# Performance work log

Measured on AMD Instinct MI355X. Metric: run time of the kernel, lower is better.

## Reference

```python
import jax, jax.numpy as jnp
import numpy as np

B, N = 256, 65536          # batch, num_tokens (world.num_tokens == N)
VOCAB = 50257
ALPHA = 0.5                # dirichlet concentration
EPS = 1e-7                 # gumbel eps


def setup_inputs() -> dict:
    key = jax.random.key(0)
    kb, kt, ku, kd = jax.random.split(key, 4)
    batch = jax.random.randint(kb, (B, N), 0, VOCAB, dtype=jnp.int32)
    t = jax.random.uniform(kt, (B,), dtype=jnp.float32)
    U = jax.random.uniform(ku, (B, N), dtype=jnp.float32)
    # dirichlet(alpha=0.5) sample over the token axis, one simplex per row
    D = jax.random.dirichlet(kd, ALPHA * jnp.ones((N,), jnp.float32), shape=(B,)).astype(jnp.float32)
    return {"batch": batch, "t": t, "U": U, "D": D}


def cosine_schedule(t):
    return 1.0 - jnp.cos(jnp.pi * t / 2)


def cosine_weight(t, eps=1e-3):
    t_adj = t * (1 - 2 * eps) + eps
    return 0.5 * jnp.pi * jnp.sin(jnp.pi * t_adj / 2)


def binary_topk(weights, ks):
    # weights: [B, N] float; ks: [B, 1] int -> bool mask marking the top-k per row
    Bn, Nn = weights.shape
    idx = jnp.argsort(-weights, axis=-1)                     # descending order indices
    rank = jnp.broadcast_to(jnp.arange(Nn), (Bn, Nn))        # rank of each sorted slot
    mask = jnp.zeros((Bn, Nn), dtype=bool)
    mask = mask.at[jnp.arange(Bn)[:, None], idx].set(ks > rank)
    return mask


def reference(batch, t, U, D):
    r = cosine_schedule(t)                                   # mask rate per sample [B]
    w = cosine_weight(t)                                     # loss weight per sample [B]
    G = -jnp.log(-jnp.log(U + EPS) + EPS)                    # gumbel noise [B, N]
    weights = G + jnp.log(D)                                 # gumbel + log-dirichlet
    ks = (N * r).astype(jnp.int32)[:, None]                  # [B, 1] tokens to mask
    mask = binary_topk(weights, ks)                          # [B, N] bool
    return mask, w
```

## Files before the change

kernel.cpp:

```cpp
#include <hip/hip_runtime.h>
#include <math.h>

#define BB 256
#define NN 65536
#define NT 1024
#define CAP 6144
#define MARGIN 2e-3f

typedef float f32x4 __attribute__((ext_vector_type(4)));

__device__ __forceinline__ unsigned int f2sort(float f) {
    unsigned int b = __float_as_uint(f);
    return (b & 0x80000000u) ? ~b : (b | 0x80000000u);
}
__device__ __forceinline__ float sort2f(unsigned int u) {
    unsigned int b = (u & 0x80000000u) ? (u & 0x7fffffffu) : ~u;
    return __uint_as_float(b);
}

__device__ __forceinline__ unsigned int wexact(float u, float d) {
    float t1 = u + 1e-7f;
    float t2 = (float)log((double)t1);
    float t3 = (-t2) + 1e-7f;
    float G  = -(float)log((double)t3);
    float lgD = (float)log((double)d);
    return f2sort(G + lgD);
}

__device__ __forceinline__ unsigned int wfast(float u, float d) {
    float t1 = u + 1e-7f;
    float t3 = -__logf(t1) + 1e-7f;
    float G  = -__logf(t3);
    return f2sort(G + __logf(d));
}

__device__ __forceinline__ bool finite_f(float f) {
    return (__float_as_uint(f) & 0x7f800000u) != 0x7f800000u;
}

#define CHUNKS(OP) OP(0) OP(1) OP(2) OP(3) OP(4) OP(5) OP(6) OP(7) \
                   OP(8) OP(9) OP(10) OP(11) OP(12) OP(13) OP(14) OP(15)

#define PASS1SEL(KKV) \
    { const int b0 = tid * 8; unsigned int cs = 0; \
      _Pragma("unroll") for (int i = 0; i < 8; i++) cs += hist[b0 + i]; \
      chunkSum[tid] = cs; } \
    __syncthreads(); \
    if (tid < 64) { \
        const int c0i = lane * 16; unsigned int s = 0; \
        _Pragma("unroll") for (int i = 0; i < 16; i++) s += chunkSum[c0i + i]; \
        unsigned int suf = s; \
        _Pragma("unroll") for (int off = 1; off < 64; off <<= 1) { \
            unsigned int tv = __shfl_down(suf, off); if (lane + off < 64) suf += tv; } \
        unsigned int above = suf - s; \
        if (suf >= (KKV) && above < (KKV)) { \
            unsigned int cum = above; \
            for (int ci = c0i + 15; ci >= c0i; ci--) { \
                unsigned int cch = chunkSum[ci]; \
                if (cum + cch >= (KKV)) { \
                    for (int b = ci * 8 + 7; ; b--) { \
                        unsigned int c2 = hist[b]; \
                        if (cum + c2 >= (KKV)) { s_sel = (unsigned int)b; s_kneed = (KKV) - cum; s_eq = c2; break; } \
                        cum += c2; } \
                    break; } \
                cum += cch; } } } \
    __syncthreads();

#define PASS2SEL(P, KN) \
    if (tid < 64) { \
        const int c0i = lane * 16; unsigned int s = 0; \
        _Pragma("unroll") for (int i = 0; i < 16; i++) s += hist[c0i + i]; \
        unsigned int suf = s; \
        _Pragma("unroll") for (int off = 1; off < 64; off <<= 1) { \
            unsigned int tv = __shfl_down(suf, off); if (lane + off < 64) suf += tv; } \
        unsigned int above = suf - s; \
        if (suf >= (KN) && above < (KN)) { \
            unsigned int cum = above; \
            for (int b = c0i + 15; ; b--) { \
                unsigned int c2 = hist[b]; \
                if (cum + c2 >= (KN)) { s_sel = ((P) << 10) | (unsigned int)b; s_kneed = (KN) - cum; s_eq = c2; break; } \
                cum += c2; } } } \
    __syncthreads();

#define PASS3SEL(P, KN) \
    if (tid < 64) { \
        const int c0i = lane * 8; unsigned int s = 0; \
        _Pragma("unroll") for (int i = 0; i < 8; i++) s += hist[c0i + i]; \
        unsigned int suf = s; \
        _Pragma("unroll") for (int off = 1; off < 64; off <<= 1) { \
            unsigned int tv = __shfl_down(suf, off); if (lane + off < 64) suf += tv; } \
        unsigned int above = suf - s; \
        if (suf >= (KN) && above < (KN)) { \
            unsigned int cum = above; \
            for (int b = c0i + 7; ; b--) { \
                unsigned int c2 = hist[b]; \
                if (cum + c2 >= (KN)) { s_sel = ((P) << 9) | (unsigned int)b; s_kneed = (KN) - cum; s_eq = c2; break; } \
                cum += c2; } } } \
    __syncthreads();

__global__ __launch_bounds__(NT, 4)
void md_fused_kernel(const float* __restrict__ Tt,
                     const float* __restrict__ U,
                     const float* __restrict__ D,
                     float* __restrict__ out,
                     float* __restrict__ wout) {
    const int row = blockIdx.x;
    const int tid = threadIdx.x;
    const int lane = tid & 63;

    const float* Ur = U + (size_t)row * NN;
    const float* Dr = D + (size_t)row * NN;
    float* Or = out + (size_t)row * NN;

    __shared__ unsigned int hist[8192];
    __shared__ unsigned int chunkSum[NT];
    __shared__ unsigned int bandU[CAP];
    __shared__ int bandIdx[CAP];
    __shared__ int s_tielist[1024];
    __shared__ unsigned int s_sel, s_kneed, s_eq;
    __shared__ int s_A, s_bandCnt, s_tiecnt, s_tieidx;

    const float t = Tt[row];
    const float pf = (float)M_PI;
    float aa = pf * t;
    float bbv = aa * 0.5f;
    float c0 = (float)cos((double)bbv);
    float r  = 1.0f - c0;
    const int k = (int)(65536.0f * r);
    if (tid == 0) {
        float tadj = t * 0.998f + 0.001f;
        float arg  = (pf * tadj) * 0.5f;
        wout[row] = (float)(0.5 * M_PI) * (float)sin((double)arg);
    }

    if (k <= 0 || k >= NN) {
        const float fill = (k >= NN) ? 1.0f : 0.0f;
        f32x4 f4 = {fill, fill, fill, fill};
        for (int j = 0; j < 16; j++)
            __builtin_nontemporal_store(f4, (f32x4*)(Or + j * 4096 + tid * 4));
        return;
    }
    const unsigned int kk = (unsigned int)k;

    uint4 v0, v1, v2, v3, v4, v5, v6, v7, v8, v9, v10, v11, v12, v13, v14, v15;

    for (int i = tid; i < 8192; i += NT) hist[i] = 0;
    if (tid == 0) { s_A = 0; s_bandCnt = 0; }
    __syncthreads();

#define COMPF(J) { \
        int e = (J) * 4096 + tid * 4; \
        float4 u4 = *(const float4*)(Ur + e); \
        float4 d4 = *(const float4*)(Dr + e); \
        v##J.x = wfast(u4.x, d4.x); \
        v##J.y = wfast(u4.y, d4.y); \
        v##J.z = wfast(u4.z, d4.z); \
        v##J.w = wfast(u4.w, d4.w); \
        atomicAdd(&hist[v##J.x >> 19], 1u); \
        atomicAdd(&hist[v##J.y >> 19], 1u); \
        atomicAdd(&hist[v##J.z >> 19], 1u); \
        atomicAdd(&hist[v##J.w >> 19], 1u); }
    CHUNKS(COMPF)
#undef COMPF
    __syncthreads();

    PASS1SEL(kk)
    const unsigned int p13 = s_sel;
    const unsigned int kn1 = s_kneed;
    hist[tid] = 0;
    __syncthreads();
#define P2F(J) { \
        if ((v##J.x >> 19) == p13) atomicAdd(&hist[(v##J.x >> 9) & 1023u], 1u); \
        if ((v##J.y >> 19) == p13) atomicAdd(&hist[(v##J.y >> 9) & 1023u], 1u); \
        if ((v##J.z >> 19) == p13) atomicAdd(&hist[(v##J.z >> 9) & 1023u], 1u); \
        if ((v##J.w >> 19) == p13) atomicAdd(&hist[(v##J.w >> 9) & 1023u], 1u); }
    CHUNKS(P2F)
#undef P2F
    __syncthreads();
    PASS2SEL(p13, kn1)

    const unsigned int p23 = s_sel;
    const float loF = sort2f(p23 << 9) - MARGIN;
    const float hiF = sort2f((p23 << 9) | 511u) + MARGIN;
    const bool badBand = !(finite_f(loF) && finite_f(hiF));
    const unsigned int lo_u = f2sort(loF);
    const unsigned int hi_u = f2sort(hiF);

    {
        int cnt = 0;
#define MRG1(J, C, CI, MF) { const unsigned int uu = v##J.C; \
        const bool din = uu > hi_u; cnt += (int)din; MF = din ? 1.0f : 0.0f; \
        if (!din && uu >= lo_u) { \
            int slot = atomicAdd(&s_bandCnt, 1); \
            if (slot < CAP) bandIdx[slot] = (J) * 4096 + tid * 4 + (CI); } }
#define MRG(J) { const int e = (J) * 4096 + tid * 4; f32x4 m; \
        MRG1(J, x, 0, m.x) MRG1(J, y, 1, m.y) MRG1(J, z, 2, m.z) MRG1(J, w, 3, m.w) \
        __builtin_nontemporal_store(m, (f32x4*)(Or + e)); }
        CHUNKS(MRG)
#undef MRG
#undef MRG1
#pragma unroll
        for (int off = 32; off >= 1; off >>= 1) cnt += __shfl_down(cnt, off);
        if (lane == 0) atomicAdd(&s_A, cnt);
    }
    __syncthreads();

    const int bandCnt = s_bandCnt;
    const int kb = k - s_A;
    const bool fallback = badBand || (bandCnt > CAP) || (kb < 0) || (kb > bandCnt);

    if (!fallback) {
        for (int j = tid; j < bandCnt; j += NT) {
            int idx = bandIdx[j];
            bandU[j] = wexact(Ur[idx], Dr[idx]);
        }
        __syncthreads();
        for (int j = tid; j < bandCnt; j += NT) {
            unsigned int me = bandU[j];
            int mi = bandIdx[j];
            int rk = 0;
            for (int i = 0; i < bandCnt; i++) {
                unsigned int o = bandU[i];
                rk += (int)((o > me) || (o == me && bandIdx[i] < mi));
            }
            if (rk < kb) Or[mi] = 1.0f;
        }
        return;
    }

    __syncthreads();
    for (int i = tid; i < 8192; i += NT) hist[i] = 0;
    __syncthreads();
#define COMPE(J) { \
        int e = (J) * 4096 + tid * 4; \
        float4 u4 = *(const float4*)(Ur + e); \
        float4 d4 = *(const float4*)(Dr + e); \
        v##J.x = wexact(u4.x, d4.x); \
        v##J.y = wexact(u4.y, d4.y); \
        v##J.z = wexact(u4.z, d4.z); \
        v##J.w = wexact(u4.w, d4.w); \
        atomicAdd(&hist[v##J.x >> 19], 1u); \
        atomicAdd(&hist[v##J.y >> 19], 1u); \
        atomicAdd(&hist[v##J.z >> 19], 1u); \
        atomicAdd(&hist[v##J.w >> 19], 1u); }
    CHUNKS(COMPE)
#undef COMPE
    __syncthreads();

    PASS1SEL(kk)
    const unsigned int q13 = s_sel;
    const unsigned int en1 = s_kneed;
    hist[tid] = 0;
    __syncthreads();
#define P2E(J) { \
        if ((v##J.x >> 19) == q13) atomicAdd(&hist[(v##J.x >> 9) & 1023u], 1u); \
        if ((v##J.y >> 19) == q13) atomicAdd(&hist[(v##J.y >> 9) & 1023u], 1u); \
        if ((v##J.z >> 19) == q13) atomicAdd(&hist[(v##J.z >> 9) & 1023u], 1u); \
        if ((v##J.w >> 19) == q13) atomicAdd(&hist[(v##J.w >> 9) & 1023u], 1u); }
    CHUNKS(P2E)
#undef P2E
    __syncthreads();
    PASS2SEL(q13, en1)

    const unsigned int q23 = s_sel;
    const unsigned int en2 = s_kneed;
    if (tid < 512) hist[tid] = 0;
    __syncthreads();
#define P3E(J) { \
        if ((v##J.x >> 9) == q23) atomicAdd(&hist[v##J.x & 511u], 1u); \
        if ((v##J.y >> 9) == q23) atomicAdd(&hist[v##J.y & 511u], 1u); \
        if ((v##J.z >> 9) == q23) atomicAdd(&hist[v##J.z & 511u], 1u); \
        if ((v##J.w >> 9) == q23) atomicAdd(&hist[v##J.w & 511u], 1u); }
    CHUNKS(P3E)
#undef P3E
    __syncthreads();
    PASS3SEL(q23, en2)

    const unsigned int theta = s_sel;
    const unsigned int kneedF = s_kneed, eqF = s_eq;
    const bool needOrder = (kneedF < eqF);
    int istar = NN;
    if (needOrder) {
        if (tid == 0) s_tiecnt = 0;
        __syncthreads();
#define TIE1(J, C, CI) if (v##J.C == theta) { \
            int pos = atomicAdd(&s_tiecnt, 1); \
            if (pos < 1024) s_tielist[pos] = (J) * 4096 + tid * 4 + (CI); }
#define TIE(J) TIE1(J, x, 0) TIE1(J, y, 1) TIE1(J, z, 2) TIE1(J, w, 3)
        CHUNKS(TIE)
#undef TIE
#undef TIE1
        __syncthreads();
        if (tid == 0) {
            int E = s_tiecnt; if (E > 1024) E = 1024;
            for (int aI = 1; aI < E; aI++) {
                int val = s_tielist[aI]; int bI = aI - 1;
                while (bI >= 0 && s_tielist[bI] > val) { s_tielist[bI + 1] = s_tielist[bI]; bI--; }
                s_tielist[bI + 1] = val;
            }
            int kk2 = (int)kneedF; if (kk2 > E) kk2 = E; if (kk2 < 1) kk2 = 1;
            s_tieidx = s_tielist[kk2 - 1];
        }
        __syncthreads();
        istar = s_tieidx;
    }

#define MVE(u, idx) ((((u) > theta) || ((u) == theta && (!needOrder || (idx) <= istar))) ? 1.0f : 0.0f)
#define WRE(J) { \
        int e = (J) * 4096 + tid * 4; \
        f32x4 m; \
        m.x = MVE(v##J.x, e + 0); \
        m.y = MVE(v##J.y, e + 1); \
        m.z = MVE(v##J.z, e + 2); \
        m.w = MVE(v##J.w, e + 3); \
        __builtin_nontemporal_store(m, (f32x4*)(Or + e)); }
    CHUNKS(WRE)
#undef WRE
#undef MVE
}

extern "C" void kernel_launch(void* const* d_in, const int* in_sizes, int n_in,
                              void* d_out, int out_size, void* d_ws, size_t ws_size,
                              hipStream_t stream) {
    const float* T = (const float*)d_in[1];
    const float* U = (const float*)d_in[2];
    const float* D = (const float*)d_in[3];
    float* out = (float*)d_out;
    float* wout = out + (size_t)BB * NN;

    md_fused_kernel<<<BB, NT, 0, stream>>>(T, U, D, out, wout);
}
```

Before: 231.7 us.

## Spill seven key chunks to LDS to cut register pressure

Keeps 7 of the 16 per-thread uint4 key chunks in shared memory instead of registers, so fewer VGPRs are live across the selection passes. The band and tie buffers are shrunk or aliased onto that shared region to stay within the LDS budget. The goal is to lower register pressure or spilling at 1024 threads per block, at the cost of extra LDS traffic on every pass and a smaller band capacity (CAP 2016), which makes the slow exact fallback path trigger more often.

```diff
diff --git a/kernel.cpp b/kernel.cpp
--- a/kernel.cpp
+++ b/kernel.cpp
@@ -4,8 +4,9 @@
 #define BB 256
 #define NN 65536
 #define NT 1024
-#define CAP 6144
+#define CAP 2016
 #define MARGIN 2e-3f
+#define NLC 7
 
 typedef float f32x4 __attribute__((ext_vector_type(4)));
 
@@ -38,8 +39,8 @@
     return (__float_as_uint(f) & 0x7f800000u) != 0x7f800000u;
 }
 
-#define CHUNKS(OP) OP(0) OP(1) OP(2) OP(3) OP(4) OP(5) OP(6) OP(7) \
-                   OP(8) OP(9) OP(10) OP(11) OP(12) OP(13) OP(14) OP(15)
+#define LCHUNKS(OP) OP(0) OP(1) OP(2) OP(3) OP(4) OP(5) OP(6)
+#define RCHUNKS(OP) OP(7) OP(8) OP(9) OP(10) OP(11) OP(12) OP(13) OP(14) OP(15)
 
 #define PASS1SEL(KKV) \
     { const int b0 = tid * 8; unsigned int cs = 0; \
@@ -112,13 +113,15 @@
     const float* Dr = D + (size_t)row * NN;
     float* Or = out + (size_t)row * NN;
 
+    __shared__ uint4 kls[NLC * 1024];
     __shared__ unsigned int hist[8192];
     __shared__ unsigned int chunkSum[NT];
-    __shared__ unsigned int bandU[CAP];
     __shared__ int bandIdx[CAP];
-    __shared__ int s_tielist[1024];
     __shared__ unsigned int s_sel, s_kneed, s_eq;
     __shared__ int s_A, s_bandCnt, s_tiecnt, s_tieidx;
+
+    unsigned int* bandU = (unsigned int*)kls;
+    int* tielist = bandIdx;
 
     const float t = Tt[row];
     const float pf = (float)M_PI;
@@ -142,13 +145,29 @@
     }
     const unsigned int kk = (unsigned int)k;
 
-    uint4 v0, v1, v2, v3, v4, v5, v6, v7, v8, v9, v10, v11, v12, v13, v14, v15;
+    uint4 v7, v8, v9, v10, v11, v12, v13, v14, v15;
 
     for (int i = tid; i < 8192; i += NT) hist[i] = 0;
     if (tid == 0) { s_A = 0; s_bandCnt = 0; }
     __syncthreads();
 
-#define COMPF(J) { \
+#define COMPFL(J) { \
+        int e = (J) * 4096 + tid * 4; \
+        float4 u4 = *(const float4*)(Ur + e); \
+        float4 d4 = *(const float4*)(Dr + e); \
+        uint4 kv; \
+        kv.x = wfast(u4.x, d4.x); \
+        kv.y = wfast(u4.y, d4.y); \
+        kv.z = wfast(u4.z, d4.z); \
+        kv.w = wfast(u4.w, d4.w); \
+        kls[(J) * 1024 + tid] = kv; \
+        atomicAdd(&hist[kv.x >> 19], 1u); \
+        atomicAdd(&hist[kv.y >> 19], 1u); \
+        atomicAdd(&hist[kv.z >> 19], 1u); \
+        atomicAdd(&hist[kv.w >> 19], 1u); }
+    LCHUNKS(COMPFL)
+#undef COMPFL
+#define COMPFR(J) { \
         int e = (J) * 4096 + tid * 4; \
         float4 u4 = *(const float4*)(Ur + e); \
         float4 d4 = *(const float4*)(Dr + e); \
@@ -160,8 +179,8 @@
         atomicAdd(&hist[v##J.y >> 19], 1u); \
         atomicAdd(&hist[v##J.z >> 19], 1u); \
         atomicAdd(&hist[v##J.w >> 19], 1u); }
-    CHUNKS(COMPF)
-#undef COMPF
+    RCHUNKS(COMPFR)
+#undef COMPFR
     __syncthreads();
 
     PASS1SEL(kk)
@@ -169,13 +188,15 @@
     const unsigned int kn1 = s_kneed;
     hist[tid] = 0;
     __syncthreads();
-#define P2F(J) { \
-        if ((v##J.x >> 19) == p13) atomicAdd(&hist[(v##J.x >> 9) & 1023u], 1u); \
-        if ((v##J.y >> 19) == p13) atomicAdd(&hist[(v##J.y >> 9) & 1023u], 1u); \
-        if ((v##J.z >> 19) == p13) atomicAdd(&hist[(v##J.z >> 9) & 1023u], 1u); \
-        if ((v##J.w >> 19) == p13) atomicAdd(&hist[(v##J.w >> 9) & 1023u], 1u); }
-    CHUNKS(P2F)
-#undef P2F
+#define P2V(UU) if (((UU) >> 19) == p13) atomicAdd(&hist[((UU) >> 9) & 1023u], 1u);
+#define P2FL(J) { const uint4 kv = kls[(J) * 1024 + tid]; \
+        P2V(kv.x) P2V(kv.y) P2V(kv.z) P2V(kv.w) }
+#define P2FR(J) { P2V(v##J.x) P2V(v##J.y) P2V(v##J.z) P2V(v##J.w) }
+    LCHUNKS(P2FL)
+    RCHUNKS(P2FR)
+#undef P2FL
+#undef P2FR
+#undef P2V
     __syncthreads();
     PASS2SEL(p13, kn1)
 
@@ -188,17 +209,25 @@
 
     {
         int cnt = 0;
-#define MRG1(J, C, CI, MF) { const unsigned int uu = v##J.C; \
+#define MRGV(UU, EIDX, MF) { const unsigned int uu = (UU); \
         const bool din = uu > hi_u; cnt += (int)din; MF = din ? 1.0f : 0.0f; \
         if (!din && uu >= lo_u) { \
             int slot = atomicAdd(&s_bandCnt, 1); \
-            if (slot < CAP) bandIdx[slot] = (J) * 4096 + tid * 4 + (CI); } }
-#define MRG(J) { const int e = (J) * 4096 + tid * 4; f32x4 m; \
-        MRG1(J, x, 0, m.x) MRG1(J, y, 1, m.y) MRG1(J, z, 2, m.z) MRG1(J, w, 3, m.w) \
+            if (slot < CAP) bandIdx[slot] = (EIDX); } }
+#define MRGL(J) { const int e = (J) * 4096 + tid * 4; \
+        const uint4 kv = kls[(J) * 1024 + tid]; f32x4 m; \
+        MRGV(kv.x, e + 0, m.x) MRGV(kv.y, e + 1, m.y) \
+        MRGV(kv.z, e + 2, m.z) MRGV(kv.w, e + 3, m.w) \
         __builtin_nontemporal_store(m, (f32x4*)(Or + e)); }
-        CHUNKS(MRG)
-#undef MRG
-#undef MRG1
+#define MRGR(J) { const int e = (J) * 4096 + tid * 4; f32x4 m; \
+        MRGV(v##J.x, e + 0, m.x) MRGV(v##J.y, e + 1, m.y) \
+        MRGV(v##J.z, e + 2, m.z) MRGV(v##J.w, e + 3, m.w) \
+        __builtin_nontemporal_store(m, (f32x4*)(Or + e)); }
+        LCHUNKS(MRGL)
+        RCHUNKS(MRGR)
+#undef MRGL
+#undef MRGR
+#undef MRGV
 #pragma unroll
         for (int off = 32; off >= 1; off >>= 1) cnt += __shfl_down(cnt, off);
         if (lane == 0) atomicAdd(&s_A, cnt);
@@ -231,7 +260,23 @@
     __syncthreads();
     for (int i = tid; i < 8192; i += NT) hist[i] = 0;
     __syncthreads();
-#define COMPE(J) { \
+#define COMPEL(J) { \
+        int e = (J) * 4096 + tid * 4; \
+        float4 u4 = *(const float4*)(Ur + e); \
+        float4 d4 = *(const float4*)(Dr + e); \
+        uint4 kv; \
+        kv.x = wexact(u4.x, d4.x); \
+        kv.y = wexact(u4.y, d4.y); \
+        kv.z = wexact(u4.z, d4.z); \
+        kv.w = wexact(u4.w, d4.w); \
+        kls[(J) * 1024 + tid] = kv; \
+        atomicAdd(&hist[kv.x >> 19], 1u); \
+        atomicAdd(&hist[kv.y >> 19], 1u); \
+        atomicAdd(&hist[kv.z >> 19], 1u); \
+        atomicAdd(&hist[kv.w >> 19], 1u); }
+    LCHUNKS(COMPEL)
+#undef COMPEL
+#define COMPER(J) { \
         int e = (J) * 4096 + tid * 4; \
         float4 u4 = *(const float4*)(Ur + e); \
         float4 d4 = *(const float4*)(Dr + e); \
@@ -243,8 +288,8 @@
         atomicAdd(&hist[v##J.y >> 19], 1u); \
         atomicAdd(&hist[v##J.z >> 19], 1u); \
         atomicAdd(&hist[v##J.w >> 19], 1u); }
-    CHUNKS(COMPE)
-#undef COMPE
+    RCHUNKS(COMPER)
+#undef COMPER
     __syncthreads();
 
     PASS1SEL(kk)
@@ -252,13 +297,15 @@
     const unsigned int en1 = s_kneed;
     hist[tid] = 0;
     __syncthreads();
-#define P2E(J) { \
-        if ((v##J.x >> 19) == q13) atomicAdd(&hist[(v##J.x >> 9) & 1023u], 1u); \
-        if ((v##J.y >> 19) == q13) atomicAdd(&hist[(v##J.y >> 9) & 1023u], 1u); \
-        if ((v##J.z >> 19) == q13) atomicAdd(&hist[(v##J.z >> 9) & 1023u], 1u); \
-        if ((v##J.w >> 19) == q13) atomicAdd(&hist[(v##J.w >> 9) & 1023u], 1u); }
-    CHUNKS(P2E)
-#undef P2E
+#define P2V(UU) if (((UU) >> 19) == q13) atomicAdd(&hist[((UU) >> 9) & 1023u], 1u);
+#define P2EL(J) { const uint4 kv = kls[(J) * 1024 + tid]; \
+        P2V(kv.x) P2V(kv.y) P2V(kv.z) P2V(kv.w) }
+#define P2ER(J) { P2V(v##J.x) P2V(v##J.y) P2V(v##J.z) P2V(v##J.w) }
+    LCHUNKS(P2EL)
+    RCHUNKS(P2ER)
+#undef P2EL
+#undef P2ER
+#undef P2V
     __syncthreads();
     PASS2SEL(q13, en1)
 
@@ -266,13 +313,15 @@
     const unsigned int en2 = s_kneed;
     if (tid < 512) hist[tid] = 0;
     __syncthreads();
-#define P3E(J) { \
-        if ((v##J.x >> 9) == q23) atomicAdd(&hist[v##J.x & 511u], 1u); \
-        if ((v##J.y >> 9) == q23) atomicAdd(&hist[v##J.y & 511u], 1u); \
-        if ((v##J.z >> 9) == q23) atomicAdd(&hist[v##J.z & 511u], 1u); \
-        if ((v##J.w >> 9) == q23) atomicAdd(&hist[v##J.w & 511u], 1u); }
-    CHUNKS(P3E)
-#undef P3E
+#define P3V(UU) if (((UU) >> 9) == q23) atomicAdd(&hist[(UU) & 511u], 1u);
+#define P3EL(J) { const uint4 kv = kls[(J) * 1024 + tid]; \
+        P3V(kv.x) P3V(kv.y) P3V(kv.z) P3V(kv.w) }
+#define P3ER(J) { P3V(v##J.x) P3V(v##J.y) P3V(v##J.z) P3V(v##J.w) }
+    LCHUNKS(P3EL)
+    RCHUNKS(P3ER)
+#undef P3EL
+#undef P3ER
+#undef P3V
     __syncthreads();
     PASS3SEL(q23, en2)
 
@@ -283,39 +332,52 @@
     if (needOrder) {
         if (tid == 0) s_tiecnt = 0;
         __syncthreads();
-#define TIE1(J, C, CI) if (v##J.C == theta) { \
+#define TIEV(UU, EIDX) if ((UU) == theta) { \
             int pos = atomicAdd(&s_tiecnt, 1); \
-            if (pos < 1024) s_tielist[pos] = (J) * 4096 + tid * 4 + (CI); }
-#define TIE(J) TIE1(J, x, 0) TIE1(J, y, 1) TIE1(J, z, 2) TIE1(J, w, 3)
-        CHUNKS(TIE)
-#undef TIE
-#undef TIE1
+            if (pos < 1024) tielist[pos] = (EIDX); }
+#define TIEL(J) { const int e = (J) * 4096 + tid * 4; \
+        const uint4 kv = kls[(J) * 1024 + tid]; \
+        TIEV(kv.x, e + 0) TIEV(kv.y, e + 1) TIEV(kv.z, e + 2) TIEV(kv.w, e + 3) }
+#define TIER(J) { const int e = (J) * 4096 + tid * 4; \
+        TIEV(v##J.x, e + 0) TIEV(v##J.y, e + 1) TIEV(v##J.z, e + 2) TIEV(v##J.w, e + 3) }
+        LCHUNKS(TIEL)
+        RCHUNKS(TIER)
+#undef TIEL
+#undef TIER
+#undef TIEV
         __syncthreads();
         if (tid == 0) {
             int E = s_tiecnt; if (E > 1024) E = 1024;
             for (int aI = 1; aI < E; aI++) {
-                int val = s_tielist[aI]; int bI = aI - 1;
-                while (bI >= 0 && s_tielist[bI] > val) { s_tielist[bI + 1] = s_tielist[bI]; bI--; }
-                s_tielist[bI + 1] = val;
+                int val = tielist[aI]; int bI = aI - 1;
+                while (bI >= 0 && tielist[bI] > val) { tielist[bI + 1] = tielist[bI]; bI--; }
+                tielist[bI + 1] = val;
             }
             int kk2 = (int)kneedF; if (kk2 > E) kk2 = E; if (kk2 < 1) kk2 = 1;
-            s_tieidx = s_tielist[kk2 - 1];
+            s_tieidx = tielist[kk2 - 1];
         }
         __syncthreads();
         istar = s_tieidx;
     }
 
 #define MVE(u, idx) ((((u) > theta) || ((u) == theta && (!needOrder || (idx) <= istar))) ? 1.0f : 0.0f)
-#define WRE(J) { \
-        int e = (J) * 4096 + tid * 4; \
-        f32x4 m; \
+#define WREL(J) { const int e = (J) * 4096 + tid * 4; \
+        const uint4 kv = kls[(J) * 1024 + tid]; f32x4 m; \
+        m.x = MVE(kv.x, e + 0); \
+        m.y = MVE(kv.y, e + 1); \
+        m.z = MVE(kv.z, e + 2); \
+        m.w = MVE(kv.w, e + 3); \
+        __builtin_nontemporal_store(m, (f32x4*)(Or + e)); }
+#define WRER(J) { const int e = (J) * 4096 + tid * 4; f32x4 m; \
         m.x = MVE(v##J.x, e + 0); \
         m.y = MVE(v##J.y, e + 1); \
         m.z = MVE(v##J.z, e + 2); \
         m.w = MVE(v##J.w, e + 3); \
         __builtin_nontemporal_store(m, (f32x4*)(Or + e)); }
-    CHUNKS(WRE)
-#undef WRE
+    LCHUNKS(WREL)
+    RCHUNKS(WRER)
+#undef WREL
+#undef WRER
 #undef MVE
 }
 
```

After: 223.4 us. 3.6% less time.

## Keep 7 of 16 key chunks in LDS and recompute the rest

Applied to the files above, without the earlier changes.

Sort keys were previously held in 64 registers per thread. Now the first 7 chunks are cached in shared memory and the other 9 are recomputed from U and D in each later pass. The band capacity shrinks and the tie list reuses the band index buffer, so the total fits in LDS. This lowers register pressure so more waves can be resident, at the cost of re-reading global memory and recomputing logs in every pass. Occupancy stays capped by the large LDS footprint, and overflowing the smaller band capacity sends more rows to the slow exact fallback.

```diff
diff --git a/kernel.cpp b/kernel.cpp
--- a/kernel.cpp
+++ b/kernel.cpp
@@ -4,8 +4,9 @@
 #define BB 256
 #define NN 65536
 #define NT 1024
-#define CAP 6144
+#define CAP 2016
 #define MARGIN 2e-3f
+#define NLC 7
 
 typedef float f32x4 __attribute__((ext_vector_type(4)));
 
@@ -37,9 +38,6 @@
 __device__ __forceinline__ bool finite_f(float f) {
     return (__float_as_uint(f) & 0x7f800000u) != 0x7f800000u;
 }
-
-#define CHUNKS(OP) OP(0) OP(1) OP(2) OP(3) OP(4) OP(5) OP(6) OP(7) \
-                   OP(8) OP(9) OP(10) OP(11) OP(12) OP(13) OP(14) OP(15)
 
 #define PASS1SEL(KKV) \
     { const int b0 = tid * 8; unsigned int cs = 0; \
@@ -112,13 +110,15 @@
     const float* Dr = D + (size_t)row * NN;
     float* Or = out + (size_t)row * NN;
 
+    __shared__ uint4 kls[NLC * 1024];
     __shared__ unsigned int hist[8192];
     __shared__ unsigned int chunkSum[NT];
-    __shared__ unsigned int bandU[CAP];
     __shared__ int bandIdx[CAP];
-    __shared__ int s_tielist[1024];
     __shared__ unsigned int s_sel, s_kneed, s_eq;
     __shared__ int s_A, s_bandCnt, s_tiecnt, s_tieidx;
+
+    unsigned int* bandU = (unsigned int*)kls;
+    int* tielist = bandIdx;
 
     const float t = Tt[row];
     const float pf = (float)M_PI;
@@ -142,26 +142,26 @@
     }
     const unsigned int kk = (unsigned int)k;
 
-    uint4 v0, v1, v2, v3, v4, v5, v6, v7, v8, v9, v10, v11, v12, v13, v14, v15;
-
     for (int i = tid; i < 8192; i += NT) hist[i] = 0;
     if (tid == 0) { s_A = 0; s_bandCnt = 0; }
     __syncthreads();
 
-#define COMPF(J) { \
-        int e = (J) * 4096 + tid * 4; \
-        float4 u4 = *(const float4*)(Ur + e); \
-        float4 d4 = *(const float4*)(Dr + e); \
-        v##J.x = wfast(u4.x, d4.x); \
-        v##J.y = wfast(u4.y, d4.y); \
-        v##J.z = wfast(u4.z, d4.z); \
-        v##J.w = wfast(u4.w, d4.w); \
-        atomicAdd(&hist[v##J.x >> 19], 1u); \
-        atomicAdd(&hist[v##J.y >> 19], 1u); \
-        atomicAdd(&hist[v##J.z >> 19], 1u); \
-        atomicAdd(&hist[v##J.w >> 19], 1u); }
-    CHUNKS(COMPF)
-#undef COMPF
+#pragma unroll 2
+    for (int J = 0; J < 16; ++J) {
+        const int e = (J << 12) + (tid << 2);
+        float4 u4 = *(const float4*)(Ur + e);
+        float4 d4 = *(const float4*)(Dr + e);
+        uint4 kv;
+        kv.x = wfast(u4.x, d4.x);
+        kv.y = wfast(u4.y, d4.y);
+        kv.z = wfast(u4.z, d4.z);
+        kv.w = wfast(u4.w, d4.w);
+        if (J < NLC) kls[(J << 10) + tid] = kv;
+        atomicAdd(&hist[kv.x >> 19], 1u);
+        atomicAdd(&hist[kv.y >> 19], 1u);
+        atomicAdd(&hist[kv.z >> 19], 1u);
+        atomicAdd(&hist[kv.w >> 19], 1u);
+    }
     __syncthreads();
 
     PASS1SEL(kk)
@@ -169,13 +169,26 @@
     const unsigned int kn1 = s_kneed;
     hist[tid] = 0;
     __syncthreads();
-#define P2F(J) { \
-        if ((v##J.x >> 19) == p13) atomicAdd(&hist[(v##J.x >> 9) & 1023u], 1u); \
-        if ((v##J.y >> 19) == p13) atomicAdd(&hist[(v##J.y >> 9) & 1023u], 1u); \
-        if ((v##J.z >> 19) == p13) atomicAdd(&hist[(v##J.z >> 9) & 1023u], 1u); \
-        if ((v##J.w >> 19) == p13) atomicAdd(&hist[(v##J.w >> 9) & 1023u], 1u); }
-    CHUNKS(P2F)
-#undef P2F
+
+#pragma unroll 2
+    for (int J = 0; J < 16; ++J) {
+        uint4 kv;
+        if (J < NLC) {
+            kv = kls[(J << 10) + tid];
+        } else {
+            const int e = (J << 12) + (tid << 2);
+            float4 u4 = *(const float4*)(Ur + e);
+            float4 d4 = *(const float4*)(Dr + e);
+            kv.x = wfast(u4.x, d4.x);
+            kv.y = wfast(u4.y, d4.y);
+            kv.z = wfast(u4.z, d4.z);
+            kv.w = wfast(u4.w, d4.w);
+        }
+        if ((kv.x >> 19) == p13) atomicAdd(&hist[(kv.x >> 9) & 1023u], 1u);
+        if ((kv.y >> 19) == p13) atomicAdd(&hist[(kv.y >> 9) & 1023u], 1u);
+        if ((kv.z >> 19) == p13) atomicAdd(&hist[(kv.z >> 9) & 1023u], 1u);
+        if ((kv.w >> 19) == p13) atomicAdd(&hist[(kv.w >> 9) & 1023u], 1u);
+    }
     __syncthreads();
     PASS2SEL(p13, kn1)
 
@@ -188,17 +201,33 @@
 
     {
         int cnt = 0;
-#define MRG1(J, C, CI, MF) { const unsigned int uu = v##J.C; \
-        const bool din = uu > hi_u; cnt += (int)din; MF = din ? 1.0f : 0.0f; \
-        if (!din && uu >= lo_u) { \
-            int slot = atomicAdd(&s_bandCnt, 1); \
-            if (slot < CAP) bandIdx[slot] = (J) * 4096 + tid * 4 + (CI); } }
-#define MRG(J) { const int e = (J) * 4096 + tid * 4; f32x4 m; \
-        MRG1(J, x, 0, m.x) MRG1(J, y, 1, m.y) MRG1(J, z, 2, m.z) MRG1(J, w, 3, m.w) \
-        __builtin_nontemporal_store(m, (f32x4*)(Or + e)); }
-        CHUNKS(MRG)
-#undef MRG
-#undef MRG1
+#pragma unroll 2
+        for (int J = 0; J < 16; ++J) {
+            const int e = (J << 12) + (tid << 2);
+            uint4 kv;
+            if (J < NLC) {
+                kv = kls[(J << 10) + tid];
+            } else {
+                float4 u4 = *(const float4*)(Ur + e);
+                float4 d4 = *(const float4*)(Dr + e);
+                kv.x = wfast(u4.x, d4.x);
+                kv.y = wfast(u4.y, d4.y);
+                kv.z = wfast(u4.z, d4.z);
+                kv.w = wfast(u4.w, d4.w);
+            }
+            f32x4 m;
+#define MRGV(UU, EIDX, MF) { const unsigned int uu = (UU); \
+            const bool din = uu > hi_u; cnt += (int)din; MF = din ? 1.0f : 0.0f; \
+            if (!din && uu >= lo_u) { \
+                int slot = atomicAdd(&s_bandCnt, 1); \
+                if (slot < CAP) bandIdx[slot] = (EIDX); } }
+            MRGV(kv.x, e + 0, m.x)
+            MRGV(kv.y, e + 1, m.y)
+            MRGV(kv.z, e + 2, m.z)
+            MRGV(kv.w, e + 3, m.w)
+#undef MRGV
+            __builtin_nontemporal_store(m, (f32x4*)(Or + e));
+        }
 #pragma unroll
         for (int off = 32; off >= 1; off >>= 1) cnt += __shfl_down(cnt, off);
         if (lane == 0) atomicAdd(&s_A, cnt);
@@ -231,20 +260,22 @@
     __syncthreads();
     for (int i = tid; i < 8192; i += NT) hist[i] = 0;
     __syncthreads();
-#define COMPE(J) { \
-        int e = (J) * 4096 + tid * 4; \
-        float4 u4 = *(const float4*)(Ur + e); \
-        float4 d4 = *(const float4*)(Dr + e); \
-        v##J.x = wexact(u4.x, d4.x); \
-        v##J.y = wexact(u4.y, d4.y); \
-        v##J.z = wexact(u4.z, d4.z); \
-        v##J.w = wexact(u4.w, d4.w); \
-        atomicAdd(&hist[v##J.x >> 19], 1u); \
-        atomicAdd(&hist[v##J.y >> 19], 1u); \
-        atomicAdd(&hist[v##J.z >> 19], 1u); \
-        atomicAdd(&hist[v##J.w >> 19], 1u); }
-    CHUNKS(COMPE)
-#undef COMPE
+#pragma unroll 1
+    for (int J = 0; J < 16; ++J) {
+        const int e = (J << 12) + (tid << 2);
+        float4 u4 = *(const float4*)(Ur + e);
+        float4 d4 = *(const float4*)(Dr + e);
+        uint4 kv;
+        kv.x = wexact(u4.x, d4.x);
+        kv.y = wexact(u4.y, d4.y);
+        kv.z = wexact(u4.z, d4.z);
+        kv.w = wexact(u4.w, d4.w);
+        if (J < NLC) kls[(J << 10) + tid] = kv;
+        atomicAdd(&hist[kv.x >> 19], 1u);
+        atomicAdd(&hist[kv.y >> 19], 1u);
+        atomicAdd(&hist[kv.z >> 19], 1u);
+        atomicAdd(&hist[kv.w >> 19], 1u);
+    }
     __syncthreads();
 
     PASS1SEL(kk)
@@ -252,13 +283,25 @@
     const unsigned int en1 = s_kneed;
     hist[tid] = 0;
     __syncthreads();
-#define P2E(J) { \
-        if ((v##J.x >> 19) == q13) atomicAdd(&hist[(v##J.x >> 9) & 1023u], 1u); \
-        if ((v##J.y >> 19) == q13) atomicAdd(&hist[(v##J.y >> 9) & 1023u], 1u); \
-        if ((v##J.z >> 19) == q13) atomicAdd(&hist[(v##J.z >> 9) & 1023u], 1u); \
-        if ((v##J.w >> 19) == q13) atomicAdd(&hist[(v##J.w >> 9) & 1023u], 1u); }
-    CHUNKS(P2E)
-#undef P2E
+#pragma unroll 1
+    for (int J = 0; J < 16; ++J) {
+        uint4 kv;
+        if (J < NLC) {
+            kv = kls[(J << 10) + tid];
+        } else {
+            const int e = (J << 12) + (tid << 2);
+            float4 u4 = *(const float4*)(Ur + e);
+            float4 d4 = *(const float4*)(Dr + e);
+            kv.x = wexact(u4.x, d4.x);
+            kv.y = wexact(u4.y, d4.y);
+            kv.z = wexact(u4.z, d4.z);
+            kv.w = wexact(u4.w, d4.w);
+        }
+        if ((kv.x >> 19) == q13) atomicAdd(&hist[(kv.x >> 9) & 1023u], 1u);
+        if ((kv.y >> 19) == q13) atomicAdd(&hist[(kv.y >> 9) & 1023u], 1u);
+        if ((kv.z >> 19) == q13) atomicAdd(&hist[(kv.z >> 9) & 1023u], 1u);
+        if ((kv.w >> 19) == q13) atomicAdd(&hist[(kv.w >> 9) & 1023u], 1u);
+    }
     __syncthreads();
     PASS2SEL(q13, en1)
 
@@ -266,13 +309,25 @@
     const unsigned int en2 = s_kneed;
     if (tid < 512) hist[tid] = 0;
     __syncthreads();
-#define P3E(J) { \
-        if ((v##J.x >> 9) == q23) atomicAdd(&hist[v##J.x & 511u], 1u); \
-        if ((v##J.y >> 9) == q23) atomicAdd(&hist[v##J.y & 511u], 1u); \
-        if ((v##J.z >> 9) == q23) atomicAdd(&hist[v##J.z & 511u], 1u); \
-        if ((v##J.w >> 9) == q23) atomicAdd(&hist[v##J.w & 511u], 1u); }
-    CHUNKS(P3E)
-#undef P3E
+#pragma unroll 1
+    for (int J = 0; J < 16; ++J) {
+        uint4 kv;
+        if (J < NLC) {
+            kv = kls[(J << 10) + tid];
+        } else {
+            const int e = (J << 12) + (tid << 2);
+            float4 u4 = *(const float4*)(Ur + e);
+            float4 d4 = *(const float4*)(Dr + e);
+            kv.x = wexact(u4.x, d4.x);
+            kv.y = wexact(u4.y, d4.y);
+            kv.z = wexact(u4.z, d4.z);
+            kv.w = wexact(u4.w, d4.w);
+        }
+        if ((kv.x >> 9) == q23) atomicAdd(&hist[kv.x & 511u], 1u);
+        if ((kv.y >> 9) == q23) atomicAdd(&hist[kv.y & 511u], 1u);
+        if ((kv.z >> 9) == q23) atomicAdd(&hist[kv.z & 511u], 1u);
+        if ((kv.w >> 9) == q23) atomicAdd(&hist[kv.w & 511u], 1u);
+    }
     __syncthreads();
     PASS3SEL(q23, en2)
 
@@ -283,40 +338,67 @@
     if (needOrder) {
         if (tid == 0) s_tiecnt = 0;
         __syncthreads();
-#define TIE1(J, C, CI) if (v##J.C == theta) { \
-            int pos = atomicAdd(&s_tiecnt, 1); \
-            if (pos < 1024) s_tielist[pos] = (J) * 4096 + tid * 4 + (CI); }
-#define TIE(J) TIE1(J, x, 0) TIE1(J, y, 1) TIE1(J, z, 2) TIE1(J, w, 3)
-        CHUNKS(TIE)
-#undef TIE
-#undef TIE1
+#pragma unroll 1
+        for (int J = 0; J < 16; ++J) {
+            const int e = (J << 12) + (tid << 2);
+            uint4 kv;
+            if (J < NLC) {
+                kv = kls[(J << 10) + tid];
+            } else {
+                float4 u4 = *(const float4*)(Ur + e);
+                float4 d4 = *(const float4*)(Dr + e);
+                kv.x = wexact(u4.x, d4.x);
+                kv.y = wexact(u4.y, d4.y);
+                kv.z = wexact(u4.z, d4.z);
+                kv.w = wexact(u4.w, d4.w);
+            }
+#define TIEV(UU, EIDX) if ((UU) == theta) { \
+                int pos = atomicAdd(&s_tiecnt, 1); \
+                if (pos < 1024) tielist[pos] = (EIDX); }
+            TIEV(kv.x, e + 0)
+            TIEV(kv.y, e + 1)
+            TIEV(kv.z, e + 2)
+            TIEV(kv.w, e + 3)
+#undef TIEV
+        }
         __syncthreads();
         if (tid == 0) {
             int E = s_tiecnt; if (E > 1024) E = 1024;
             for (int aI = 1; aI < E; aI++) {
-                int val = s_tielist[aI]; int bI = aI - 1;
-                while (bI >= 0 && s_tielist[bI] > val) { s_tielist[bI + 1] = s_tielist[bI]; bI--; }
-                s_tielist[bI + 1] = val;
+                int val = tielist[aI]; int bI = aI - 1;
+                while (bI >= 0 && tielist[bI] > val) { tielist[bI + 1] = tielist[bI]; bI--; }
+                tielist[bI + 1] = val;
             }
             int kk2 = (int)kneedF; if (kk2 > E) kk2 = E; if (kk2 < 1) kk2 = 1;
-            s_tieidx = s_tielist[kk2 - 1];
+            s_tieidx = tielist[kk2 - 1];
         }
         __syncthreads();
         istar = s_tieidx;
     }
 
+#pragma unroll 1
+    for (int J = 0; J < 16; ++J) {
+        const int e = (J << 12) + (tid << 2);
+        uint4 kv;
+        if (J < NLC) {
+            kv = kls[(J << 10) + tid];
+        } else {
+            float4 u4 = *(const float4*)(Ur + e);
+            float4 d4 = *(const float4*)(Dr + e);
+            kv.x = wexact(u4.x, d4.x);
+            kv.y = wexact(u4.y, d4.y);
+            kv.z = wexact(u4.z, d4.z);
+            kv.w = wexact(u4.w, d4.w);
+        }
+        f32x4 m;
 #define MVE(u, idx) ((((u) > theta) || ((u) == theta && (!needOrder || (idx) <= istar))) ? 1.0f : 0.0f)
-#define WRE(J) { \
-        int e = (J) * 4096 + tid * 4; \
-        f32x4 m; \
-        m.x = MVE(v##J.x, e + 0); \
-        m.y = MVE(v##J.y, e + 1); \
-        m.z = MVE(v##J.z, e + 2); \
-        m.w = MVE(v##J.w, e + 3); \
-        __builtin_nontemporal_store(m, (f32x4*)(Or + e)); }
-    CHUNKS(WRE)
-#undef WRE
+        m.x = MVE(kv.x, e + 0);
+        m.y = MVE(kv.y, e + 1);
+        m.z = MVE(kv.z, e + 2);
+        m.w = MVE(kv.w, e + 3);
 #undef MVE
+        __builtin_nontemporal_store(m, (f32x4*)(Or + e));
+    }
 }
 
 extern "C" void kernel_launch(void* const* d_in, const int* in_sizes, int n_in,
```

Result: slower. 241.5 us (+4.2%).
